# Kernel optimization log

Hardware: AMD Instinct MI355X
Metric: run time of the kernel (lower is better)

The kernel has to match this reference:

```python
import jax, jax.numpy as jnp
import numpy as np

N, E = 20000, 160000
NFEAT, NHID, NCLASS = 512, 256, 64


def _unif(key, shape):
    s = 1.0 / np.sqrt(shape[-1])
    return jax.random.uniform(key, shape, jnp.float32, -s, s)


def setup_inputs() -> dict:
    key = jax.random.key(0)
    ks = jax.random.split(key, 16)
    return {
        "x": jax.random.normal(ks[0], (N, NFEAT), jnp.float32),
        "edge_index": jax.random.randint(ks[1], (2, E), 0, N, dtype=jnp.int32).astype(jnp.int64),
        "head": 0,
        # Relation 1 (nfeat -> nfeat)
        "r1_g1": _unif(ks[2], (NFEAT, NFEAT)),
        "r1_g2": _unif(ks[3], (NFEAT, NFEAT)),
        "r1_b1": _unif(ks[4], (NFEAT, NFEAT)),
        "r1_b2": _unif(ks[5], (NFEAT, NFEAT)),
        "r1_m": _unif(ks[6], (1, NFEAT)),
        "gc1_w": _unif(ks[7], (NHID, NFEAT)),   # GCNConv.lin.weight [out,in]
        "gc1_b": jnp.zeros((NHID,), jnp.float32),
        # Relation 2 (nhid -> nhid)
        "r2_g1": _unif(ks[8], (NHID, NHID)),
        "r2_g2": _unif(ks[9], (NHID, NHID)),
        "r2_b1": _unif(ks[10], (NHID, NHID)),
        "r2_b2": _unif(ks[11], (NHID, NHID)),
        "r2_m": _unif(ks[12], (1, NHID)),
        "gc2_w": _unif(ks[13], (NCLASS, NHID)),
        "gc2_b": jnp.zeros((NCLASS,), jnp.float32),
    }


def _scatter_mean(vals, idx, n):
    s = jax.ops.segment_sum(vals, idx, num_segments=n)
    c = jax.ops.segment_sum(jnp.ones(idx.shape, vals.dtype), idx, num_segments=n)
    return s / jnp.clip(c, 1.0)[:, None]


def _relation(ft, nb, g1, g2, b1, b2, m):
    # gamma/beta FiLM-style modulation, then TransE-style translation
    gamma = jax.nn.leaky_relu(ft @ g1.T + nb @ g2.T, 0.2) + 1.0
    beta = jax.nn.leaky_relu(ft @ b1.T + nb @ b2.T, 0.2)
    return ft + (gamma * m + beta) - nb


def _gcn(x, edge_index, w, b):
    # PyG GCNConv with add_self_loops=True, symmetric normalization
    n = x.shape[0]
    h = x @ w.T
    loop = jnp.arange(n, dtype=edge_index.dtype)
    row = jnp.concatenate([edge_index[0], loop])
    col = jnp.concatenate([edge_index[1], loop])
    deg = jax.ops.segment_sum(jnp.ones(col.shape, h.dtype), col, num_segments=n)
    dinv = jnp.where(deg > 0, deg ** -0.5, 0.0)
    norm = dinv[row] * dinv[col]
    out = jax.ops.segment_sum(norm[:, None] * h[row], col, num_segments=n)
    return out + b


def _trans_gcn(x, edge_index, rg1, rg2, rb1, rb2, rm, gw, gb, head):
    row, col = edge_index[0], edge_index[1]
    n = x.shape[0]
    num_nb = jax.ops.segment_sum(jnp.ones(row.shape, x.dtype), row, num_segments=n)
    nb = _scatter_mean(x[col], row, n)
    output = _relation(x, nb, rg1, rg2, rb1, rb2, rm)
    h_k = _gcn(x, edge_index, gw, gb)
    if not head:  # tail branch (ablation=0: h_s = output)
        h_s = output @ gw.T
        h_k = (h_k + h_s) / (num_nb + 1.0)[:, None]
    return h_k, output


def reference(x, edge_index, head, r1_g1, r1_g2, r1_b1, r1_b2, r1_m, gc1_w, gc1_b,
              r2_g1, r2_g2, r2_b1, r2_b2, r2_m, gc2_w, gc2_b):
    x1, out1 = _trans_gcn(x, edge_index, r1_g1, r1_g2, r1_b1, r1_b2, r1_m, gc1_w, gc1_b, head)
    x1 = jax.nn.elu(x1)  # dropout is identity in eval mode
    x2, out2 = _trans_gcn(x1, edge_index, r2_g1, r2_g2, r2_b1, r2_b2, r2_m, gc2_w, gc2_b, head)
    return (x2, jax.nn.log_softmax(x2, axis=1), out1, out2)
```

## Files before the change

### kernel.cpp

```cpp
#include <hip/hip_runtime.h>
#include <hip/hip_bf16.h>
#include <stdint.h>

typedef __bf16 bf16;
typedef __attribute__((ext_vector_type(8))) __bf16 bf16x8;
typedef __attribute__((ext_vector_type(4))) float f32x4;

#define NNODE 20000
#define NEDGE 160000
#define NFEATD 512
#define NHIDD 256
#define NCLSD 64

__device__ __forceinline__ void async_copy16(const bf16* g, bf16* l) {
  __builtin_amdgcn_global_load_lds((__attribute__((address_space(1))) void*)g,
                                   (__attribute__((address_space(3))) void*)l,
                                   16, 0, 0);
}

struct GemmArgs {
  const bf16 *A1, *A2, *W1, *W2, *zpage;
  int ldA, ldW, K1, Ktot, Nvalid, ldC, Nrows, Arows, Wrows;
  bf16* outB;
  float* outF;
  float* outF2;
  const float* mrow;
  const float* Xf;
  const bf16* Xh;
  const bf16* nbm;
  float* outG;
  bf16* outB2;
  const float* agg;
  const bf16* hself;
  int hld;
  const float* dinv;
  const float* bias;
  const float* rnb;
  int elu;
  const bf16* Wh;
  int ldWh, Wrowsh, Kh, Nintmain;
};

template <int MODE>
__global__ __launch_bounds__(256) void gemm_bt(GemmArgs ga) {
  __shared__ bf16 sA[2][128 * 64];
  __shared__ bf16 sB[2][128 * 64];
  const int tid = threadIdx.x;
  const int lane = tid & 63;
  const int w = tid >> 6;
  const int wm = w >> 1, wn = w & 1;

  const int gx = gridDim.x;
  const int nwg = gx * gridDim.y;
  const int orig = blockIdx.y * gx + blockIdx.x;
  const int qq = nwg >> 3, rm = nwg & 7;
  const int xcd = orig & 7, sidx = orig >> 3;
  const int wg = (xcd < rm ? xcd * (qq + 1) : rm * (qq + 1) + (xcd - rm) * qq) + sidx;
  const int bn0 = (wg % gx) * 128;
  const int bm0 = (wg / gx) * 128;

  const bool isH = (MODE == 2) && ga.Wh && (bn0 >= ga.Nintmain);
  const bf16* Wp1 = isH ? ga.Wh : ga.W1;
  const bf16* Wp2 = isH ? ga.Wh : ga.W2;
  const int ldW = isH ? ga.ldWh : ga.ldW;
  const int Wrows = isH ? ga.Wrowsh : ga.Wrows;
  const int bn0L = isH ? bn0 - ga.Nintmain : bn0;
  const int nt1 = (isH ? ga.Kh : ga.K1) >> 6;
  const int nt = (isH ? ga.Kh : ga.Ktot) >> 6;

  const int srow = tid >> 3;
  const int scol = (((tid & 7) ^ (srow & 7)) << 3);
  const bf16* zp = ga.zpage + tid * 8;
  int offA[4], offB[4];
  bool okA[4], okB[4];
#pragma unroll
  for (int r = 0; r < 4; r++) {
    const int ra = bm0 + r * 32 + srow;
    const int rb = bn0L + r * 32 + srow;
    okA[r] = ra < ga.Arows;
    okB[r] = rb < Wrows;
    offA[r] = ra * ga.ldA + scol;
    offB[r] = rb * ldW + scol;
  }

  auto stage = [&](int t, int p) {
    const int seg = t >= nt1;
    const int koff = (t - (seg ? nt1 : 0)) << 6;
    const bf16* As = seg ? ga.A2 : ga.A1;
    const bf16* Ws = seg ? Wp2 : Wp1;
    bf16* dA = &sA[p][tid * 8];
    bf16* dB = &sB[p][tid * 8];
#pragma unroll
    for (int r = 0; r < 4; r++)
      async_copy16(okA[r] ? As + offA[r] + koff : zp, dA + r * 2048);
#pragma unroll
    for (int r = 0; r < 4; r++)
      async_copy16(okB[r] ? Ws + offB[r] + koff : zp, dB + r * 2048);
  };

  const int sl = lane >> 4;
  const int rAb = wm * 64 + (lane & 15);
  const int rBb = wn * 64 + (lane & 15);
  const int a7 = rAb & 7, b7 = rBb & 7;

  f32x4 acc[4][4] = {};

  stage(0, 0);
  stage(1, 1);
  asm volatile("s_waitcnt vmcnt(8)" ::: "memory");
  __builtin_amdgcn_s_barrier();
  asm volatile("" ::: "memory");

  for (int t = 0; t < nt; ++t) {
    const int p = t & 1;
    const bf16* pA = &sA[p][0];
    const bf16* pB = &sB[p][0];
    bf16x8 af[4][2], bv[4][2];
#pragma unroll
    for (int mi = 0; mi < 4; mi++)
#pragma unroll
      for (int kk = 0; kk < 2; kk++)
        af[mi][kk] = *(const bf16x8*)((const char*)pA + (rAb + mi * 16) * 128 +
                                      ((((kk << 2) + sl) ^ a7) << 4));
#pragma unroll
    for (int ni = 0; ni < 4; ni++)
#pragma unroll
      for (int kk = 0; kk < 2; kk++)
        bv[ni][kk] = *(const bf16x8*)((const char*)pB + (rBb + ni * 16) * 128 +
                                      ((((kk << 2) + sl) ^ b7) << 4));
    if (t + 2 < nt) {
      asm volatile("s_waitcnt lgkmcnt(0)" ::: "memory");
      __builtin_amdgcn_s_barrier();
      asm volatile("" ::: "memory");
      stage(t + 2, p);
    }
    __builtin_amdgcn_s_setprio(1);
#pragma unroll
    for (int mi = 0; mi < 4; mi++)
#pragma unroll
      for (int ni = 0; ni < 4; ni++)
#pragma unroll
        for (int kk = 0; kk < 2; kk++)
          acc[mi][ni] =
              __builtin_amdgcn_mfma_f32_16x16x32_bf16(af[mi][kk], bv[ni][kk], acc[mi][ni], 0, 0, 0);
    __builtin_amdgcn_s_setprio(0);
    if (t + 1 < nt) {
      if (t + 2 < nt) asm volatile("s_waitcnt vmcnt(8)" ::: "memory");
      else            asm volatile("s_waitcnt vmcnt(0)" ::: "memory");
      __builtin_amdgcn_s_barrier();
      asm volatile("" ::: "memory");
    }
  }

  if constexpr (MODE == 0) {
    const int Nv = ga.Nvalid;
#pragma unroll
    for (int mi = 0; mi < 4; mi++) {
      const int rb = bm0 + wm * 64 + mi * 16 + ((lane >> 4) << 2);
#pragma unroll
      for (int ni = 0; ni < 4; ni++) {
        const int c = bn0 + wn * 64 + ni * 16 + (lane & 15);
#pragma unroll
        for (int i = 0; i < 4; i++) {
          const int r = rb + i;
          if (r < ga.Nrows && c < Nv) ga.outB[(size_t)r * ga.ldC + c] = (bf16)acc[mi][ni][i];
        }
      }
    }
  } else if constexpr (MODE == 2) {
    if (isH) {
#pragma unroll
      for (int mi = 0; mi < 4; mi++) {
        const int rb = bm0 + wm * 64 + mi * 16 + ((lane >> 4) << 2);
#pragma unroll
        for (int ni = 0; ni < 4; ni++) {
          const int c = bn0L + wn * 64 + ni * 16 + (lane & 15);
#pragma unroll
          for (int i = 0; i < 4; i++) {
            const int r = rb + i;
            if (r < ga.Nrows && c < ga.ldC) ga.outB[(size_t)r * ga.ldC + c] = (bf16)acc[mi][ni][i];
          }
        }
      }
    } else {
      const int Dr = ga.Nvalid;
      const int Lb = ((bn0 + wn * 64) >> 1) + (lane & 15);
#pragma unroll
      for (int mi = 0; mi < 4; mi++) {
        const int rb = bm0 + wm * 64 + mi * 16 + ((lane >> 4) << 2);
#pragma unroll
        for (int p = 0; p < 2; p++) {
          const int L = Lb + p * 16;
          const float mv = ga.mrow[L];
#pragma unroll
          for (int i = 0; i < 4; i++) {
            const int r = rb + i;
            if (r >= ga.Nrows) continue;
            const size_t idx = (size_t)r * Dr + L;
            float vg = acc[mi][2 * p][i];
            float vb = acc[mi][2 * p + 1][i];
            float gamma = (vg > 0.f ? vg : 0.2f * vg) + 1.0f;
            float beta = vb > 0.f ? vb : 0.2f * vb;
            float ft = ga.Xf ? ga.Xf[idx] : (float)ga.Xh[idx];
            float o = ft + gamma * mv + beta - (float)ga.nbm[idx];
            ga.outG[idx] = o;
            ga.outB2[idx] = (bf16)o;
          }
        }
      }
    }
  } else if constexpr (MODE == 3) {
    const int Nv = ga.Nvalid;
#pragma unroll
    for (int mi = 0; mi < 4; mi++) {
      const int rb = bm0 + wm * 64 + mi * 16 + ((lane >> 4) << 2);
#pragma unroll
      for (int ni = 0; ni < 4; ni++) {
        const int c = bn0 + wn * 64 + ni * 16 + (lane & 15);
#pragma unroll
        for (int i = 0; i < 4; i++) {
          const int r = rb + i;
          if (r >= ga.Nrows || c >= Nv) continue;
          const size_t idx = (size_t)r * ga.ldC + c;
          float dv = ga.dinv[r];
          float hs = (float)ga.hself[(size_t)r * ga.hld + c];
          float hv = (ga.agg[idx] + dv * dv * hs + ga.bias[c] + acc[mi][ni][i]) * ga.rnb[r];
          if (ga.elu) hv = hv > 0.f ? hv : expm1f(hv);
          ga.outB[idx] = (bf16)hv;
        }
      }
    }
  } else {
    if (wn == 0) {
#pragma unroll
      for (int mi = 0; mi < 4; mi++) {
        const int rb = bm0 + wm * 64 + mi * 16 + ((lane >> 4) << 2);
#pragma unroll
        for (int i = 0; i < 4; i++) {
          const int r = rb + i;
          const bool ok = r < ga.Nrows;
          float dv = ok ? ga.dinv[r] : 0.f;
          float rn = ok ? ga.rnb[r] : 1.f;
          float hv[4];
#pragma unroll
          for (int ni = 0; ni < 4; ni++) {
            const int c = ni * 16 + (lane & 15);
            float hs = ok ? (float)ga.hself[(size_t)r * ga.hld + c] : 0.f;
            float ag = ok ? ga.agg[(size_t)r * 64 + c] : 0.f;
            hv[ni] = ok ? (ag + dv * dv * hs + ga.bias[c] + acc[mi][ni][i]) * rn : 0.f;
          }
          float mx = fmaxf(fmaxf(hv[0], hv[1]), fmaxf(hv[2], hv[3]));
          mx = fmaxf(mx, __shfl_xor(mx, 1));
          mx = fmaxf(mx, __shfl_xor(mx, 2));
          mx = fmaxf(mx, __shfl_xor(mx, 4));
          mx = fmaxf(mx, __shfl_xor(mx, 8));
          float s = expf(hv[0] - mx) + expf(hv[1] - mx) + expf(hv[2] - mx) + expf(hv[3] - mx);
          s += __shfl_xor(s, 1);
          s += __shfl_xor(s, 2);
          s += __shfl_xor(s, 4);
          s += __shfl_xor(s, 8);
          float ls = logf(s);
          if (ok) {
#pragma unroll
            for (int ni = 0; ni < 4; ni++) {
              const int c = ni * 16 + (lane & 15);
              ga.outF[(size_t)r * 64 + c] = hv[ni];
              ga.outF2[(size_t)r * 64 + c] = hv[ni] - mx - ls;
            }
          }
        }
      }
    }
  }
}

#define PREP_NB0 10000
#define PREP_NB1 10128
#define PREP_NB2 10144
#define PREP_NB3 11168
#define PREP_NB4 11424
#define PREP_NB5 11589

__device__ __forceinline__ void cvt4(const float* __restrict__ src, bf16* __restrict__ dst,
                                     int i) {
  float4 v = *(const float4*)(src + i);
  union { bf16 b[4]; uint2 u; } o;
  o.b[0] = (bf16)v.x; o.b[1] = (bf16)v.y; o.b[2] = (bf16)v.z; o.b[3] = (bf16)v.w;
  *(uint2*)(dst + i) = o.u;
}

__device__ __forceinline__ void relw4(const float* __restrict__ g1, const float* __restrict__ g2,
                                      const float* __restrict__ b1, const float* __restrict__ b2,
                                      bf16* __restrict__ dst, int D, int idx) {
  int R = idx / (2 * D), C = idx % (2 * D);
  int q = R >> 5, s = R & 31;
  int sr = q * 16 + (s & 15);
  const float* src = (s < 16) ? ((C < D) ? g1 : g2) : ((C < D) ? b1 : b2);
  int cc = (C < D) ? C : C - D;
  float4 v = *(const float4*)(src + (size_t)sr * D + cc);
  union { bf16 b[4]; uint2 u; } o;
  o.b[0] = (bf16)v.x; o.b[1] = (bf16)v.y; o.b[2] = (bf16)v.z; o.b[3] = (bf16)v.w;
  *(uint2*)(dst + (size_t)R * 2 * D + C) = o.u;
}

__global__ __launch_bounds__(256) void prep_all(
    const float* __restrict__ x, const float* __restrict__ gc1w, const float* __restrict__ gc2w,
    const float* __restrict__ r1g1, const float* __restrict__ r1g2,
    const float* __restrict__ r1b1, const float* __restrict__ r1b2,
    const float* __restrict__ r2g1, const float* __restrict__ r2g2,
    const float* __restrict__ r2b1, const float* __restrict__ r2b2,
    bf16* __restrict__ xb, bf16* __restrict__ wgc1, bf16* __restrict__ wgc2,
    bf16* __restrict__ Wrel1, bf16* __restrict__ Wrel2,
    int* __restrict__ icr, int* __restrict__ icc, int* __restrict__ zpage) {
  const int b = blockIdx.x;
  const int tid = threadIdx.x;
  if (b < PREP_NB0) {
    cvt4(x, xb, (b * 256 + tid) * 4);
  } else if (b < PREP_NB1) {
    cvt4(gc1w, wgc1, ((b - PREP_NB0) * 256 + tid) * 4);
  } else if (b < PREP_NB2) {
    cvt4(gc2w, wgc2, ((b - PREP_NB1) * 256 + tid) * 4);
  } else if (b < PREP_NB3) {
    relw4(r1g1, r1g2, r1b1, r1b2, Wrel1, 512, ((b - PREP_NB2) * 256 + tid) * 4);
  } else if (b < PREP_NB4) {
    relw4(r2g1, r2g2, r2b1, r2b2, Wrel2, 256, ((b - PREP_NB3) * 256 + tid) * 4);
  } else {
    int i = (b - PREP_NB4) * 256 + tid;
    if (i < NNODE) icr[i] = 0;
    else if (i < 2 * NNODE) icc[i - NNODE] = 0;
    else if (i < 2 * NNODE + 2048) zpage[i - 2 * NNODE] = 0;
  }
}

__global__ void count_int(const int* __restrict__ ei, int* cr, int* cc, int E) {
  int e = blockIdx.x * 256 + threadIdx.x;
  if (e < E) {
    atomicAdd(&cr[ei[e]], 1);
    atomicAdd(&cc[ei[E + e]], 1);
  }
}

__global__ void scan_excl2(const int* __restrict__ cr, const int* __restrict__ cc,
                           int* __restrict__ rptr, int* __restrict__ cptr,
                           int* __restrict__ curr, int* __restrict__ curc,
                           float* __restrict__ nbscale, float* __restrict__ rnb,
                           float* __restrict__ dinv, int n) {
  int t = threadIdx.x;
  {
    int b0 = blockIdx.x * (n / 2);
    for (int j = b0 + t; j < b0 + n / 2; j += 256) {
      float a = (float)cr[j];
      nbscale[j] = 1.0f / fmaxf(a, 1.0f);
      rnb[j] = 1.0f / (a + 1.0f);
      dinv[j] = rsqrtf((float)cc[j] + 1.0f);
    }
  }
  const int* cnt = blockIdx.x ? cc : cr;
  int* ptr = blockIdx.x ? cptr : rptr;
  int* cur = blockIdx.x ? curc : curr;
  __shared__ int part[256];
  int chunk = (n + 255) / 256;
  int base = t * chunk;
  int s = 0;
  for (int i = 0; i < chunk; i++) {
    int j = base + i;
    if (j < n) s += cnt[j];
  }
  part[t] = s;
  __syncthreads();
  if (t == 0) {
    int r = 0;
    for (int i = 0; i < 256; i++) { int v = part[i]; part[i] = r; r += v; }
    ptr[n] = r;
  }
  __syncthreads();
  int run = part[t];
  for (int i = 0; i < chunk; i++) {
    int j = base + i;
    if (j < n) {
      ptr[j] = run;
      cur[j] = run;
      run += cnt[j];
    }
  }
}

__global__ void csr_fill(const int* __restrict__ ei, int* cur_r, int* cur_c,
                         int* __restrict__ adj_r, int* __restrict__ adj_c, int E) {
  int e = blockIdx.x * 256 + threadIdx.x;
  if (e >= E) return;
  int row = ei[e], col = ei[E + e];
  int p = atomicAdd(&cur_r[row], 1);
  adj_r[p] = col;
  int q = atomicAdd(&cur_c[col], 1);
  adj_c[q] = row;
}

__global__ void spmm_nb1(const int* __restrict__ rowptr, const int* __restrict__ adj,
                         const bf16* __restrict__ x, const float* __restrict__ nbscale,
                         bf16* __restrict__ nbp, int n) {
  int r = blockIdx.x * 4 + (threadIdx.x >> 6);
  if (r >= n) return;
  int lane = threadIdx.x & 63;
  int e0 = rowptr[r], e1 = rowptr[r + 1];
  float a[8] = {0.f, 0.f, 0.f, 0.f, 0.f, 0.f, 0.f, 0.f};
  int e = e0;
  for (; e + 8 <= e1; e += 8) {
    union { uint4 u; bf16 b[8]; } v[8];
    int ix[8];
#pragma unroll
    for (int k = 0; k < 8; k++) ix[k] = adj[e + k];
#pragma unroll
    for (int k = 0; k < 8; k++) v[k].u = *(const uint4*)(x + (size_t)ix[k] * NFEATD + lane * 8);
#pragma unroll
    for (int j = 0; j < 8; j++) {
      float t = 0.f;
#pragma unroll
      for (int k = 0; k < 8; k++) t += (float)v[k].b[j];
      a[j] += t;
    }
  }
  for (; e + 4 <= e1; e += 4) {
    int i0 = adj[e], i1 = adj[e + 1], i2 = adj[e + 2], i3 = adj[e + 3];
    union { uint4 u; bf16 b[8]; } v0, v1, v2, v3;
    v0.u = *(const uint4*)(x + (size_t)i0 * NFEATD + lane * 8);
    v1.u = *(const uint4*)(x + (size_t)i1 * NFEATD + lane * 8);
    v2.u = *(const uint4*)(x + (size_t)i2 * NFEATD + lane * 8);
    v3.u = *(const uint4*)(x + (size_t)i3 * NFEATD + lane * 8);
#pragma unroll
    for (int j = 0; j < 8; j++)
      a[j] += (float)v0.b[j] + (float)v1.b[j] + (float)v2.b[j] + (float)v3.b[j];
  }
  for (; e < e1; e++) {
    union { uint4 u; bf16 b[8]; } v;
    v.u = *(const uint4*)(x + (size_t)adj[e] * NFEATD + lane * 8);
#pragma unroll
    for (int j = 0; j < 8; j++) a[j] += (float)v.b[j];
  }
  float s = nbscale[r];
  union { bf16 b[8]; uint4 u; } o;
#pragma unroll
  for (int j = 0; j < 8; j++) o.b[j] = (bf16)(a[j] * s);
  *(uint4*)(nbp + (size_t)r * NFEATD + lane * 8) = o.u;
}

__global__ void spmm_nb2(const int* __restrict__ rowptr, const int* __restrict__ adj,
                         const bf16* __restrict__ x, const float* __restrict__ nbscale,
                         bf16* __restrict__ nbp, int n) {
  int r = blockIdx.x * 4 + (threadIdx.x >> 6);
  if (r >= n) return;
  int lane = threadIdx.x & 63;
  int e0 = rowptr[r], e1 = rowptr[r + 1];
  float a[4] = {0.f, 0.f, 0.f, 0.f};
  int e = e0;
  for (; e + 8 <= e1; e += 8) {
    union { uint2 u; bf16 b[4]; } v[8];
    int ix[8];
#pragma unroll
    for (int k = 0; k < 8; k++) ix[k] = adj[e + k];
#pragma unroll
    for (int k = 0; k < 8; k++) v[k].u = *(const uint2*)(x + (size_t)ix[k] * NHIDD + lane * 4);
#pragma unroll
    for (int j = 0; j < 4; j++) {
      float t = 0.f;
#pragma unroll
      for (int k = 0; k < 8; k++) t += (float)v[k].b[j];
      a[j] += t;
    }
  }
  for (; e + 4 <= e1; e += 4) {
    int i0 = adj[e], i1 = adj[e + 1], i2 = adj[e + 2], i3 = adj[e + 3];
    union { uint2 u; bf16 b[4]; } v0, v1, v2, v3;
    v0.u = *(const uint2*)(x + (size_t)i0 * NHIDD + lane * 4);
    v1.u = *(const uint2*)(x + (size_t)i1 * NHIDD + lane * 4);
    v2.u = *(const uint2*)(x + (size_t)i2 * NHIDD + lane * 4);
    v3.u = *(const uint2*)(x + (size_t)i3 * NHIDD + lane * 4);
#pragma unroll
    for (int j = 0; j < 4; j++)
      a[j] += (float)v0.b[j] + (float)v1.b[j] + (float)v2.b[j] + (float)v3.b[j];
  }
  for (; e < e1; e++) {
    union { uint2 u; bf16 b[4]; } v;
    v.u = *(const uint2*)(x + (size_t)adj[e] * NHIDD + lane * 4);
#pragma unroll
    for (int j = 0; j < 4; j++) a[j] += (float)v.b[j];
  }
  float s = nbscale[r];
  union { bf16 b[4]; uint2 u; } o;
#pragma unroll
  for (int j = 0; j < 4; j++) o.b[j] = (bf16)(a[j] * s);
  *(uint2*)(nbp + (size_t)r * NHIDD + lane * 4) = o.u;
}

__global__ void spmm_gcn256(const int* __restrict__ colptr, const int* __restrict__ adj,
                            const bf16* __restrict__ h, int hld, const float* __restrict__ dinv,
                            float* __restrict__ agg, int n) {
  int c = blockIdx.x * 4 + (threadIdx.x >> 6);
  if (c >= n) return;
  int lane = threadIdx.x & 63;
  int e0 = colptr[c], e1 = colptr[c + 1];
  float a[4] = {0.f, 0.f, 0.f, 0.f};
  int e = e0;
  for (; e + 4 <= e1; e += 4) {
    int i0 = adj[e], i1 = adj[e + 1], i2 = adj[e + 2], i3 = adj[e + 3];
    float w0 = dinv[i0], w1 = dinv[i1], w2 = dinv[i2], w3 = dinv[i3];
    union { uint2 u; bf16 b[4]; } v0, v1, v2, v3;
    v0.u = *(const uint2*)(h + (size_t)i0 * hld + lane * 4);
    v1.u = *(const uint2*)(h + (size_t)i1 * hld + lane * 4);
    v2.u = *(const uint2*)(h + (size_t)i2 * hld + lane * 4);
    v3.u = *(const uint2*)(h + (size_t)i3 * hld + lane * 4);
#pragma unroll
    for (int j = 0; j < 4; j++)
      a[j] += w0 * (float)v0.b[j] + w1 * (float)v1.b[j] + w2 * (float)v2.b[j] + w3 * (float)v3.b[j];
  }
  for (; e < e1; e++) {
    int rr = adj[e];
    float wv = dinv[rr];
    union { uint2 u; bf16 b[4]; } v;
    v.u = *(const uint2*)(h + (size_t)rr * hld + lane * 4);
#pragma unroll
    for (int j = 0; j < 4; j++) a[j] += wv * (float)v.b[j];
  }
  float wc = dinv[c];
  f32x4 o;
#pragma unroll
  for (int j = 0; j < 4; j++) o[j] = a[j] * wc;
  *(f32x4*)(agg + (size_t)c * NHIDD + lane * 4) = o;
}

__global__ void spmm_gcn64(const int* __restrict__ colptr, const int* __restrict__ adj,
                           const bf16* __restrict__ h, int hld, const float* __restrict__ dinv,
                           float* __restrict__ agg, int n) {
  int c = blockIdx.x * 4 + (threadIdx.x >> 6);
  if (c >= n) return;
  int lane = threadIdx.x & 63;
  int e0 = colptr[c], e1 = colptr[c + 1];
  float a = 0.f;
  int e = e0;
  for (; e + 4 <= e1; e += 4) {
    int i0 = adj[e], i1 = adj[e + 1], i2 = adj[e + 2], i3 = adj[e + 3];
    float h0 = (float)h[(size_t)i0 * hld + lane];
    float h1 = (float)h[(size_t)i1 * hld + lane];
    float h2 = (float)h[(size_t)i2 * hld + lane];
    float h3 = (float)h[(size_t)i3 * hld + lane];
    a += dinv[i0] * h0 + dinv[i1] * h1 + dinv[i2] * h2 + dinv[i3] * h3;
  }
  for (; e < e1; e++) {
    int rr = adj[e];
    a += dinv[rr] * (float)h[(size_t)rr * hld + lane];
  }
  agg[(size_t)c * NCLSD + lane] = a * dinv[c];
}

extern "C" void kernel_launch(void* const* d_in, const int* in_sizes, int n_in, void* d_out,
                              int out_size, void* d_ws, size_t ws_size, hipStream_t stream) {
  const float* x = (const float*)d_in[0];
  const int* ei = (const int*)d_in[1];
  const float* r1g1 = (const float*)d_in[3];
  const float* r1g2 = (const float*)d_in[4];
  const float* r1b1 = (const float*)d_in[5];
  const float* r1b2 = (const float*)d_in[6];
  const float* r1m = (const float*)d_in[7];
  const float* gc1w = (const float*)d_in[8];
  const float* gc1b = (const float*)d_in[9];
  const float* r2g1 = (const float*)d_in[10];
  const float* r2g2 = (const float*)d_in[11];
  const float* r2b1 = (const float*)d_in[12];
  const float* r2b2 = (const float*)d_in[13];
  const float* r2m = (const float*)d_in[14];
  const float* gc2w = (const float*)d_in[15];
  const float* gc2b = (const float*)d_in[16];
  float* out = (float*)d_out;

  char* ws = (char*)d_ws;
  size_t off = 0;
  auto alloc = [&](size_t bytes) -> char* {
    char* p = ws + off;
    off = (off + bytes + 511) & ~(size_t)511;
    return p;
  };
  float* nbscale = (float*)alloc((size_t)NNODE * 4);
  float* rnb = (float*)alloc((size_t)NNODE * 4);
  float* dinv = (float*)alloc((size_t)NNODE * 4);
  int* icr = (int*)alloc((size_t)NNODE * 4);
  int* icc = (int*)alloc((size_t)NNODE * 4);
  int* rptr = (int*)alloc((size_t)(NNODE + 1) * 4);
  int* cptr = (int*)alloc((size_t)(NNODE + 1) * 4);
  int* curr = (int*)alloc((size_t)NNODE * 4);
  int* curc = (int*)alloc((size_t)NNODE * 4);
  int* adjr = (int*)alloc((size_t)NEDGE * 4);
  int* adjc = (int*)alloc((size_t)NEDGE * 4);
  bf16* zpage = (bf16*)alloc(8192);
  bf16* Wrel1 = (bf16*)alloc((size_t)1024 * 1024 * 2);
  bf16* Wrel2 = (bf16*)alloc((size_t)512 * 512 * 2);
  bf16* wgc1 = (bf16*)alloc((size_t)NHIDD * NFEATD * 2);
  bf16* wgc2 = (bf16*)alloc((size_t)NCLSD * NHIDD * 2);
  bf16* xb = (bf16*)alloc((size_t)NNODE * NFEATD * 2);
  bf16* nbp1 = (bf16*)alloc((size_t)NNODE * NFEATD * 2);
  bf16* out1b = (bf16*)alloc((size_t)NNODE * NFEATD * 2);
  bf16* h1b = (bf16*)alloc((size_t)NNODE * NHIDD * 2);
  float* agg1 = (float*)alloc((size_t)NNODE * NHIDD * 4);
  bf16* x1b = (bf16*)alloc((size_t)NNODE * NHIDD * 2);
  bf16* nb2p = (bf16*)alloc((size_t)NNODE * NHIDD * 2);
  bf16* out2b = (bf16*)alloc((size_t)NNODE * NHIDD * 2);
  bf16* h2b = (bf16*)alloc((size_t)NNODE * NCLSD * 2);
  float* agg2 = (float*)alloc((size_t)NNODE * NCLSD * 4);

  const size_t OUT1OFF = (size_t)2 * NNODE * NCLSD;
  const size_t OUT2OFF = OUT1OFF + (size_t)NNODE * NFEATD;
  float* out1g = out + OUT1OFF;
  float* out2g = out + OUT2OFF;

  const int MB = (NNODE + 127) / 128;
  const int NW4 = (NNODE + 3) / 4;

  prep_all<<<PREP_NB5, 256, 0, stream>>>(x, gc1w, gc2w, r1g1, r1g2, r1b1, r1b2,
                                         r2g1, r2g2, r2b1, r2b2, xb, wgc1, wgc2,
                                         Wrel1, Wrel2, icr, icc, (int*)zpage);

  count_int<<<(NEDGE + 255) / 256, 256, 0, stream>>>(ei, icr, icc, NEDGE);
  scan_excl2<<<2, 256, 0, stream>>>(icr, icc, rptr, cptr, curr, curc, nbscale, rnb, dinv, NNODE);
  csr_fill<<<(NEDGE + 255) / 256, 256, 0, stream>>>(ei, curr, curc, adjr, adjc, NEDGE);

  spmm_nb1<<<NW4, 256, 0, stream>>>(rptr, adjr, xb, nbscale, nbp1, NNODE);

  GemmArgs a;
  auto base = [&](const bf16* A1, const bf16* A2, int ldA, const bf16* W1, const bf16* W2,
                  int ldW, int K1, int Kt, int Nv, int ldC, int Wr) {
    a = GemmArgs{};
    a.A1 = A1; a.A2 = A2; a.W1 = W1; a.W2 = W2; a.zpage = zpage;
    a.ldA = ldA; a.ldW = ldW; a.K1 = K1; a.Ktot = Kt; a.Nvalid = Nv; a.ldC = ldC;
    a.Nrows = NNODE; a.Arows = NNODE; a.Wrows = Wr;
  };

  base(xb, nbp1, NFEATD, Wrel1, Wrel1 + 512, 1024, NFEATD, 2 * NFEATD, NFEATD, NHIDD, 1024);
  a.mrow = r1m; a.Xf = x; a.nbm = nbp1; a.outG = out1g; a.outB2 = out1b;
  a.Wh = wgc1; a.ldWh = NFEATD; a.Wrowsh = NHIDD; a.Kh = NFEATD; a.Nintmain = 1024;
  a.outB = h1b;
  gemm_bt<2><<<dim3(10, MB), 256, 0, stream>>>(a);

  spmm_gcn256<<<NW4, 256, 0, stream>>>(cptr, adjc, h1b, NHIDD, dinv, agg1, NNODE);

  base(out1b, out1b, NFEATD, wgc1, wgc1, NFEATD, NFEATD, NFEATD, NHIDD, NHIDD, NHIDD);
  a.agg = agg1; a.hself = h1b; a.hld = NHIDD; a.dinv = dinv; a.bias = gc1b; a.rnb = rnb;
  a.elu = 1; a.outB = x1b;
  gemm_bt<3><<<dim3(2, MB), 256, 0, stream>>>(a);

  spmm_nb2<<<NW4, 256, 0, stream>>>(rptr, adjr, x1b, nbscale, nb2p, NNODE);

  base(x1b, nb2p, NHIDD, Wrel2, Wrel2 + 256, 512, NHIDD, 2 * NHIDD, NHIDD, NCLSD, 512);
  a.mrow = r2m; a.Xf = nullptr; a.Xh = x1b; a.nbm = nb2p; a.outG = out2g; a.outB2 = out2b;
  a.Wh = wgc2; a.ldWh = NHIDD; a.Wrowsh = NCLSD; a.Kh = NHIDD; a.Nintmain = 512;
  a.outB = h2b;
  gemm_bt<2><<<dim3(5, MB), 256, 0, stream>>>(a);

  spmm_gcn64<<<NW4, 256, 0, stream>>>(cptr, adjc, h2b, NCLSD, dinv, agg2, NNODE);

  base(out2b, out2b, NHIDD, wgc2, wgc2, NHIDD, NHIDD, NHIDD, NCLSD, NCLSD, NCLSD);
  a.agg = agg2; a.hself = h2b; a.hld = NCLSD; a.dinv = dinv; a.bias = gc2b; a.rnb = rnb;
  a.elu = 0; a.outF = out; a.outF2 = out + (size_t)NNODE * NCLSD;
  gemm_bt<4><<<dim3(1, MB), 256, 0, stream>>>(a);
}
```

Baseline: 493.6 us.

## Co-schedule SpMM gathers with independent GEMMs in single launches

Reorders the dependency graph so each sparse gather runs in the same launch as an independent GEMM. Extra workgroups beyond the GEMM tiles do the gather: the X@Wgc1 GEMM now runs with the first neighbour-mean gather, and the GCN aggregation of h1 runs inside the relation GEMM. The same pairing is applied in layer 2. This removes four separate launches and lets memory-bound gathers overlap compute-bound tiles, at the cost of more register pressure in one fused kernel and possible load imbalance between the two kinds of blocks.

```diff
diff --git a/kernel.cpp b/kernel.cpp
--- a/kernel.cpp
+++ b/kernel.cpp
@@ -21,6 +21,7 @@
 struct GemmArgs {
   const bf16 *A1, *A2, *W1, *W2, *zpage;
   int ldA, ldW, K1, Ktot, Nvalid, ldC, Nrows, Arows, Wrows;
+  int gxG, nGemm;
   bf16* outB;
   float* outF;
   float* outF2;
@@ -37,37 +38,166 @@
   const float* bias;
   const float* rnb;
   int elu;
-  const bf16* Wh;
-  int ldWh, Wrowsh, Kh, Nintmain;
+  const int* gptr;
+  const int* gadj;
+  const bf16* gsrc;
+  bf16* gdstB;
+  float* gdstF;
+  const float* gnbs;
 };
 
-template <int MODE>
+template <int MODE, int GM, int GW>
 __global__ __launch_bounds__(256) void gemm_bt(GemmArgs ga) {
   __shared__ bf16 sA[2][128 * 64];
   __shared__ bf16 sB[2][128 * 64];
   const int tid = threadIdx.x;
+  const int orig = blockIdx.x;
+
+  if constexpr (GM == 1) {
+    if (orig >= ga.nGemm) {
+      const int r = (orig - ga.nGemm) * 4 + (tid >> 6);
+      if (r < NNODE) {
+        const int lane = tid & 63;
+        const int e0 = ga.gptr[r], e1 = ga.gptr[r + 1];
+        if constexpr (GW == 512) {
+          float a[8] = {};
+          int e = e0;
+          for (; e + 8 <= e1; e += 8) {
+            union { uint4 u; bf16 b[8]; } v[8];
+            int ix[8];
+#pragma unroll
+            for (int k = 0; k < 8; k++) ix[k] = ga.gadj[e + k];
+#pragma unroll
+            for (int k = 0; k < 8; k++)
+              v[k].u = *(const uint4*)(ga.gsrc + (size_t)ix[k] * 512 + lane * 8);
+#pragma unroll
+            for (int j = 0; j < 8; j++) {
+              float t = 0.f;
+#pragma unroll
+              for (int k = 0; k < 8; k++) t += (float)v[k].b[j];
+              a[j] += t;
+            }
+          }
+          for (; e < e1; e++) {
+            union { uint4 u; bf16 b[8]; } v;
+            v.u = *(const uint4*)(ga.gsrc + (size_t)ga.gadj[e] * 512 + lane * 8);
+#pragma unroll
+            for (int j = 0; j < 8; j++) a[j] += (float)v.b[j];
+          }
+          float s = ga.gnbs[r];
+          union { bf16 b[8]; uint4 u; } o;
+#pragma unroll
+          for (int j = 0; j < 8; j++) o.b[j] = (bf16)(a[j] * s);
+          *(uint4*)(ga.gdstB + (size_t)r * 512 + lane * 8) = o.u;
+        } else {
+          float a[4] = {};
+          int e = e0;
+          for (; e + 8 <= e1; e += 8) {
+            union { uint2 u; bf16 b[4]; } v[8];
+            int ix[8];
+#pragma unroll
+            for (int k = 0; k < 8; k++) ix[k] = ga.gadj[e + k];
+#pragma unroll
+            for (int k = 0; k < 8; k++)
+              v[k].u = *(const uint2*)(ga.gsrc + (size_t)ix[k] * 256 + lane * 4);
+#pragma unroll
+            for (int j = 0; j < 4; j++) {
+              float t = 0.f;
+#pragma unroll
+              for (int k = 0; k < 8; k++) t += (float)v[k].b[j];
+              a[j] += t;
+            }
+          }
+          for (; e < e1; e++) {
+            union { uint2 u; bf16 b[4]; } v;
+            v.u = *(const uint2*)(ga.gsrc + (size_t)ga.gadj[e] * 256 + lane * 4);
+#pragma unroll
+            for (int j = 0; j < 4; j++) a[j] += (float)v.b[j];
+          }
+          float s = ga.gnbs[r];
+          union { bf16 b[4]; uint2 u; } o;
+#pragma unroll
+          for (int j = 0; j < 4; j++) o.b[j] = (bf16)(a[j] * s);
+          *(uint2*)(ga.gdstB + (size_t)r * 256 + lane * 4) = o.u;
+        }
+      }
+      return;
+    }
+  } else if constexpr (GM == 2) {
+    if (orig >= ga.nGemm) {
+      const int r = (orig - ga.nGemm) * 4 + (tid >> 6);
+      if (r < NNODE) {
+        const int lane = tid & 63;
+        const int e0 = ga.gptr[r], e1 = ga.gptr[r + 1];
+        if constexpr (GW == 256) {
+          float a[4] = {};
+          int e = e0;
+          for (; e + 8 <= e1; e += 8) {
+            union { uint2 u; bf16 b[4]; } v[8];
+            int ix[8];
+            float wv[8];
+#pragma unroll
+            for (int k = 0; k < 8; k++) ix[k] = ga.gadj[e + k];
+#pragma unroll
+            for (int k = 0; k < 8; k++) wv[k] = ga.dinv[ix[k]];
+#pragma unroll
+            for (int k = 0; k < 8; k++)
+              v[k].u = *(const uint2*)(ga.gsrc + (size_t)ix[k] * 256 + lane * 4);
+#pragma unroll
+            for (int j = 0; j < 4; j++) {
+              float t = 0.f;
+#pragma unroll
+              for (int k = 0; k < 8; k++) t += wv[k] * (float)v[k].b[j];
+              a[j] += t;
+            }
+          }
+          for (; e < e1; e++) {
+            int i0 = ga.gadj[e];
+            float w0 = ga.dinv[i0];
+            union { uint2 u; bf16 b[4]; } v;
+            v.u = *(const uint2*)(ga.gsrc + (size_t)i0 * 256 + lane * 4);
+#pragma unroll
+            for (int j = 0; j < 4; j++) a[j] += w0 * (float)v.b[j];
+          }
+          float wc = ga.dinv[r];
+          f32x4 o;
+#pragma unroll
+          for (int j = 0; j < 4; j++) o[j] = a[j] * wc;
+          *(f32x4*)(ga.gdstF + (size_t)r * 256 + lane * 4) = o;
+        } else {
+          float a = 0.f;
+          int e = e0;
+          for (; e + 4 <= e1; e += 4) {
+            int i0 = ga.gadj[e], i1 = ga.gadj[e + 1], i2 = ga.gadj[e + 2], i3 = ga.gadj[e + 3];
+            float h0 = (float)ga.gsrc[(size_t)i0 * 64 + lane];
+            float h1 = (float)ga.gsrc[(size_t)i1 * 64 + lane];
+            float h2 = (float)ga.gsrc[(size_t)i2 * 64 + lane];
+            float h3 = (float)ga.gsrc[(size_t)i3 * 64 + lane];
+            a += ga.dinv[i0] * h0 + ga.dinv[i1] * h1 + ga.dinv[i2] * h2 + ga.dinv[i3] * h3;
+          }
+          for (; e < e1; e++) {
+            int rr = ga.gadj[e];
+            a += ga.dinv[rr] * (float)ga.gsrc[(size_t)rr * 64 + lane];
+          }
+          ga.gdstF[(size_t)r * 64 + lane] = a * ga.dinv[r];
+        }
+      }
+      return;
+    }
+  }
+
   const int lane = tid & 63;
   const int w = tid >> 6;
   const int wm = w >> 1, wn = w & 1;
 
-  const int gx = gridDim.x;
-  const int nwg = gx * gridDim.y;
-  const int orig = blockIdx.y * gx + blockIdx.x;
+  const int gx = ga.gxG;
+  const int nwg = ga.nGemm;
   const int qq = nwg >> 3, rm = nwg & 7;
   const int xcd = orig & 7, sidx = orig >> 3;
   const int wg = (xcd < rm ? xcd * (qq + 1) : rm * (qq + 1) + (xcd - rm) * qq) + sidx;
   const int bn0 = (wg % gx) * 128;
   const int bm0 = (wg / gx) * 128;
 
-  const bool isH = (MODE == 2) && ga.Wh && (bn0 >= ga.Nintmain);
-  const bf16* Wp1 = isH ? ga.Wh : ga.W1;
-  const bf16* Wp2 = isH ? ga.Wh : ga.W2;
-  const int ldW = isH ? ga.ldWh : ga.ldW;
-  const int Wrows = isH ? ga.Wrowsh : ga.Wrows;
-  const int bn0L = isH ? bn0 - ga.Nintmain : bn0;
-  const int nt1 = (isH ? ga.Kh : ga.K1) >> 6;
-  const int nt = (isH ? ga.Kh : ga.Ktot) >> 6;
-
   const int srow = tid >> 3;
   const int scol = (((tid & 7) ^ (srow & 7)) << 3);
   const bf16* zp = ga.zpage + tid * 8;
@@ -76,18 +206,20 @@
 #pragma unroll
   for (int r = 0; r < 4; r++) {
     const int ra = bm0 + r * 32 + srow;
-    const int rb = bn0L + r * 32 + srow;
+    const int rb = bn0 + r * 32 + srow;
     okA[r] = ra < ga.Arows;
-    okB[r] = rb < Wrows;
+    okB[r] = rb < ga.Wrows;
     offA[r] = ra * ga.ldA + scol;
-    offB[r] = rb * ldW + scol;
-  }
+    offB[r] = rb * ga.ldW + scol;
+  }
+  const int nt1 = ga.K1 >> 6;
+  const int nt = ga.Ktot >> 6;
 
   auto stage = [&](int t, int p) {
     const int seg = t >= nt1;
     const int koff = (t - (seg ? nt1 : 0)) << 6;
     const bf16* As = seg ? ga.A2 : ga.A1;
-    const bf16* Ws = seg ? Wp2 : Wp1;
+    const bf16* Ws = seg ? ga.W2 : ga.W1;
     bf16* dA = &sA[p][tid * 8];
     bf16* dB = &sB[p][tid * 8];
 #pragma unroll
@@ -168,44 +300,28 @@
       }
     }
   } else if constexpr (MODE == 2) {
-    if (isH) {
-#pragma unroll
-      for (int mi = 0; mi < 4; mi++) {
-        const int rb = bm0 + wm * 64 + mi * 16 + ((lane >> 4) << 2);
-#pragma unroll
-        for (int ni = 0; ni < 4; ni++) {
-          const int c = bn0L + wn * 64 + ni * 16 + (lane & 15);
-#pragma unroll
-          for (int i = 0; i < 4; i++) {
-            const int r = rb + i;
-            if (r < ga.Nrows && c < ga.ldC) ga.outB[(size_t)r * ga.ldC + c] = (bf16)acc[mi][ni][i];
-          }
-        }
-      }
-    } else {
-      const int Dr = ga.Nvalid;
-      const int Lb = ((bn0 + wn * 64) >> 1) + (lane & 15);
-#pragma unroll
-      for (int mi = 0; mi < 4; mi++) {
-        const int rb = bm0 + wm * 64 + mi * 16 + ((lane >> 4) << 2);
-#pragma unroll
-        for (int p = 0; p < 2; p++) {
-          const int L = Lb + p * 16;
-          const float mv = ga.mrow[L];
-#pragma unroll
-          for (int i = 0; i < 4; i++) {
-            const int r = rb + i;
-            if (r >= ga.Nrows) continue;
-            const size_t idx = (size_t)r * Dr + L;
-            float vg = acc[mi][2 * p][i];
-            float vb = acc[mi][2 * p + 1][i];
-            float gamma = (vg > 0.f ? vg : 0.2f * vg) + 1.0f;
-            float beta = vb > 0.f ? vb : 0.2f * vb;
-            float ft = ga.Xf ? ga.Xf[idx] : (float)ga.Xh[idx];
-            float o = ft + gamma * mv + beta - (float)ga.nbm[idx];
-            ga.outG[idx] = o;
-            ga.outB2[idx] = (bf16)o;
-          }
+    const int Dr = ga.Nvalid;
+    const int Lb = ((bn0 + wn * 64) >> 1) + (lane & 15);
+#pragma unroll
+    for (int mi = 0; mi < 4; mi++) {
+      const int rb = bm0 + wm * 64 + mi * 16 + ((lane >> 4) << 2);
+#pragma unroll
+      for (int p = 0; p < 2; p++) {
+        const int L = Lb + p * 16;
+        const float mv = ga.mrow[L];
+#pragma unroll
+        for (int i = 0; i < 4; i++) {
+          const int r = rb + i;
+          if (r >= ga.Nrows) continue;
+          const size_t idx = (size_t)r * Dr + L;
+          float vg = acc[mi][2 * p][i];
+          float vb = acc[mi][2 * p + 1][i];
+          float gamma = (vg > 0.f ? vg : 0.2f * vg) + 1.0f;
+          float beta = vb > 0.f ? vb : 0.2f * vb;
+          float ft = ga.Xf ? ga.Xf[idx] : (float)ga.Xh[idx];
+          float o = ft + gamma * mv + beta - (float)ga.nbm[idx];
+          ga.outG[idx] = o;
+          ga.outB2[idx] = (bf16)o;
         }
       }
     }
@@ -394,162 +510,6 @@
   adj_r[p] = col;
   int q = atomicAdd(&cur_c[col], 1);
   adj_c[q] = row;
-}
-
-__global__ void spmm_nb1(const int* __restrict__ rowptr, const int* __restrict__ adj,
-                         const bf16* __restrict__ x, const float* __restrict__ nbscale,
-                         bf16* __restrict__ nbp, int n) {
-  int r = blockIdx.x * 4 + (threadIdx.x >> 6);
-  if (r >= n) return;
-  int lane = threadIdx.x & 63;
-  int e0 = rowptr[r], e1 = rowptr[r + 1];
-  float a[8] = {0.f, 0.f, 0.f, 0.f, 0.f, 0.f, 0.f, 0.f};
-  int e = e0;
-  for (; e + 8 <= e1; e += 8) {
-    union { uint4 u; bf16 b[8]; } v[8];
-    int ix[8];
-#pragma unroll
-    for (int k = 0; k < 8; k++) ix[k] = adj[e + k];
-#pragma unroll
-    for (int k = 0; k < 8; k++) v[k].u = *(const uint4*)(x + (size_t)ix[k] * NFEATD + lane * 8);
-#pragma unroll
-    for (int j = 0; j < 8; j++) {
-      float t = 0.f;
-#pragma unroll
-      for (int k = 0; k < 8; k++) t += (float)v[k].b[j];
-      a[j] += t;
-    }
-  }
-  for (; e + 4 <= e1; e += 4) {
-    int i0 = adj[e], i1 = adj[e + 1], i2 = adj[e + 2], i3 = adj[e + 3];
-    union { uint4 u; bf16 b[8]; } v0, v1, v2, v3;
-    v0.u = *(const uint4*)(x + (size_t)i0 * NFEATD + lane * 8);
-    v1.u = *(const uint4*)(x + (size_t)i1 * NFEATD + lane * 8);
-    v2.u = *(const uint4*)(x + (size_t)i2 * NFEATD + lane * 8);
-    v3.u = *(const uint4*)(x + (size_t)i3 * NFEATD + lane * 8);
-#pragma unroll
-    for (int j = 0; j < 8; j++)
-      a[j] += (float)v0.b[j] + (float)v1.b[j] + (float)v2.b[j] + (float)v3.b[j];
-  }
-  for (; e < e1; e++) {
-    union { uint4 u; bf16 b[8]; } v;
-    v.u = *(const uint4*)(x + (size_t)adj[e] * NFEATD + lane * 8);
-#pragma unroll
-    for (int j = 0; j < 8; j++) a[j] += (float)v.b[j];
-  }
-  float s = nbscale[r];
-  union { bf16 b[8]; uint4 u; } o;
-#pragma unroll
-  for (int j = 0; j < 8; j++) o.b[j] = (bf16)(a[j] * s);
-  *(uint4*)(nbp + (size_t)r * NFEATD + lane * 8) = o.u;
-}
-
-__global__ void spmm_nb2(const int* __restrict__ rowptr, const int* __restrict__ adj,
-                         const bf16* __restrict__ x, const float* __restrict__ nbscale,
-                         bf16* __restrict__ nbp, int n) {
-  int r = blockIdx.x * 4 + (threadIdx.x >> 6);
-  if (r >= n) return;
-  int lane = threadIdx.x & 63;
-  int e0 = rowptr[r], e1 = rowptr[r + 1];
-  float a[4] = {0.f, 0.f, 0.f, 0.f};
-  int e = e0;
-  for (; e + 8 <= e1; e += 8) {
-    union { uint2 u; bf16 b[4]; } v[8];
-    int ix[8];
-#pragma unroll
-    for (int k = 0; k < 8; k++) ix[k] = adj[e + k];
-#pragma unroll
-    for (int k = 0; k < 8; k++) v[k].u = *(const uint2*)(x + (size_t)ix[k] * NHIDD + lane * 4);
-#pragma unroll
-    for (int j = 0; j < 4; j++) {
-      float t = 0.f;
-#pragma unroll
-      for (int k = 0; k < 8; k++) t += (float)v[k].b[j];
-      a[j] += t;
-    }
-  }
-  for (; e + 4 <= e1; e += 4) {
-    int i0 = adj[e], i1 = adj[e + 1], i2 = adj[e + 2], i3 = adj[e + 3];
-    union { uint2 u; bf16 b[4]; } v0, v1, v2, v3;
-    v0.u = *(const uint2*)(x + (size_t)i0 * NHIDD + lane * 4);
-    v1.u = *(const uint2*)(x + (size_t)i1 * NHIDD + lane * 4);
-    v2.u = *(const uint2*)(x + (size_t)i2 * NHIDD + lane * 4);
-    v3.u = *(const uint2*)(x + (size_t)i3 * NHIDD + lane * 4);
-#pragma unroll
-    for (int j = 0; j < 4; j++)
-      a[j] += (float)v0.b[j] + (float)v1.b[j] + (float)v2.b[j] + (float)v3.b[j];
-  }
-  for (; e < e1; e++) {
-    union { uint2 u; bf16 b[4]; } v;
-    v.u = *(const uint2*)(x + (size_t)adj[e] * NHIDD + lane * 4);
-#pragma unroll
-    for (int j = 0; j < 4; j++) a[j] += (float)v.b[j];
-  }
-  float s = nbscale[r];
-  union { bf16 b[4]; uint2 u; } o;
-#pragma unroll
-  for (int j = 0; j < 4; j++) o.b[j] = (bf16)(a[j] * s);
-  *(uint2*)(nbp + (size_t)r * NHIDD + lane * 4) = o.u;
-}
-
-__global__ void spmm_gcn256(const int* __restrict__ colptr, const int* __restrict__ adj,
-                            const bf16* __restrict__ h, int hld, const float* __restrict__ dinv,
-                            float* __restrict__ agg, int n) {
-  int c = blockIdx.x * 4 + (threadIdx.x >> 6);
-  if (c >= n) return;
-  int lane = threadIdx.x & 63;
-  int e0 = colptr[c], e1 = colptr[c + 1];
-  float a[4] = {0.f, 0.f, 0.f, 0.f};
-  int e = e0;
-  for (; e + 4 <= e1; e += 4) {
-    int i0 = adj[e], i1 = adj[e + 1], i2 = adj[e + 2], i3 = adj[e + 3];
-    float w0 = dinv[i0], w1 = dinv[i1], w2 = dinv[i2], w3 = dinv[i3];
-    union { uint2 u; bf16 b[4]; } v0, v1, v2, v3;
-    v0.u = *(const uint2*)(h + (size_t)i0 * hld + lane * 4);
-    v1.u = *(const uint2*)(h + (size_t)i1 * hld + lane * 4);
-    v2.u = *(const uint2*)(h + (size_t)i2 * hld + lane * 4);
-    v3.u = *(const uint2*)(h + (size_t)i3 * hld + lane * 4);
-#pragma unroll
-    for (int j = 0; j < 4; j++)
-      a[j] += w0 * (float)v0.b[j] + w1 * (float)v1.b[j] + w2 * (float)v2.b[j] + w3 * (float)v3.b[j];
-  }
-  for (; e < e1; e++) {
-    int rr = adj[e];
-    float wv = dinv[rr];
-    union { uint2 u; bf16 b[4]; } v;
-    v.u = *(const uint2*)(h + (size_t)rr * hld + lane * 4);
-#pragma unroll
-    for (int j = 0; j < 4; j++) a[j] += wv * (float)v.b[j];
-  }
-  float wc = dinv[c];
-  f32x4 o;
-#pragma unroll
-  for (int j = 0; j < 4; j++) o[j] = a[j] * wc;
-  *(f32x4*)(agg + (size_t)c * NHIDD + lane * 4) = o;
-}
-
-__global__ void spmm_gcn64(const int* __restrict__ colptr, const int* __restrict__ adj,
-                           const bf16* __restrict__ h, int hld, const float* __restrict__ dinv,
-                           float* __restrict__ agg, int n) {
-  int c = blockIdx.x * 4 + (threadIdx.x >> 6);
-  if (c >= n) return;
-  int lane = threadIdx.x & 63;
-  int e0 = colptr[c], e1 = colptr[c + 1];
-  float a = 0.f;
-  int e = e0;
-  for (; e + 4 <= e1; e += 4) {
-    int i0 = adj[e], i1 = adj[e + 1], i2 = adj[e + 2], i3 = adj[e + 3];
-    float h0 = (float)h[(size_t)i0 * hld + lane];
-    float h1 = (float)h[(size_t)i1 * hld + lane];
-    float h2 = (float)h[(size_t)i2 * hld + lane];
-    float h3 = (float)h[(size_t)i3 * hld + lane];
-    a += dinv[i0] * h0 + dinv[i1] * h1 + dinv[i2] * h2 + dinv[i3] * h3;
-  }
-  for (; e < e1; e++) {
-    int rr = adj[e];
-    a += dinv[rr] * (float)h[(size_t)rr * hld + lane];
-  }
-  agg[(size_t)c * NCLSD + lane] = a * dinv[c];
 }
 
 extern "C" void kernel_launch(void* const* d_in, const int* in_sizes, int n_in, void* d_out,
@@ -622,8 +582,6 @@
   scan_excl2<<<2, 256, 0, stream>>>(icr, icc, rptr, cptr, curr, curc, nbscale, rnb, dinv, NNODE);
   csr_fill<<<(NEDGE + 255) / 256, 256, 0, stream>>>(ei, curr, curc, adjr, adjc, NEDGE);
 
-  spmm_nb1<<<NW4, 256, 0, stream>>>(rptr, adjr, xb, nbscale, nbp1, NNODE);
-
   GemmArgs a;
   auto base = [&](const bf16* A1, const bf16* A2, int ldA, const bf16* W1, const bf16* W2,
                   int ldW, int K1, int Kt, int Nv, int ldC, int Wr) {
@@ -633,31 +591,36 @@
     a.Nrows = NNODE; a.Arows = NNODE; a.Wrows = Wr;
   };
 
-  base(xb, nbp1, NFEATD, Wrel1, Wrel1 + 512, 1024, NFEATD, 2 * NFEATD, NFEATD, NHIDD, 1024);
+  base(xb, xb, NFEATD, wgc1, wgc1, NFEATD, NFEATD, NFEATD, NHIDD, NHIDD, NHIDD);
+  a.outB = h1b; a.gxG = 2; a.nGemm = 2 * MB;
+  a.gptr = rptr; a.gadj = adjr; a.gsrc = xb; a.gdstB = nbp1; a.gnbs = nbscale;
+  gemm_bt<0, 1, 512><<<2 * MB + NW4, 256, 0, stream>>>(a);
+
+  base(xb, nbp1, NFEATD, Wrel1, Wrel1 + 512, 1024, NFEATD, 2 * NFEATD, NFEATD, NFEATD, 1024);
   a.mrow = r1m; a.Xf = x; a.nbm = nbp1; a.outG = out1g; a.outB2 = out1b;
-  a.Wh = wgc1; a.ldWh = NFEATD; a.Wrowsh = NHIDD; a.Kh = NFEATD; a.Nintmain = 1024;
-  a.outB = h1b;
-  gemm_bt<2><<<dim3(10, MB), 256, 0, stream>>>(a);
-
-  spmm_gcn256<<<NW4, 256, 0, stream>>>(cptr, adjc, h1b, NHIDD, dinv, agg1, NNODE);
+  a.gxG = 8; a.nGemm = 8 * MB;
+  a.gptr = cptr; a.gadj = adjc; a.gsrc = h1b; a.gdstF = agg1; a.dinv = dinv;
+  gemm_bt<2, 2, 256><<<8 * MB + NW4, 256, 0, stream>>>(a);
 
   base(out1b, out1b, NFEATD, wgc1, wgc1, NFEATD, NFEATD, NFEATD, NHIDD, NHIDD, NHIDD);
   a.agg = agg1; a.hself = h1b; a.hld = NHIDD; a.dinv = dinv; a.bias = gc1b; a.rnb = rnb;
-  a.elu = 1; a.outB = x1b;
-  gemm_bt<3><<<dim3(2, MB), 256, 0, stream>>>(a);
-
-  spmm_nb2<<<NW4, 256, 0, stream>>>(rptr, adjr, x1b, nbscale, nb2p, NNODE);
-
-  base(x1b, nb2p, NHIDD, Wrel2, Wrel2 + 256, 512, NHIDD, 2 * NHIDD, NHIDD, NCLSD, 512);
+  a.elu = 1; a.outB = x1b; a.gxG = 2; a.nGemm = 2 * MB;
+  gemm_bt<3, 0, 0><<<2 * MB, 256, 0, stream>>>(a);
+
+  base(x1b, x1b, NHIDD, wgc2, wgc2, NHIDD, NHIDD, NHIDD, NCLSD, NCLSD, NCLSD);
+  a.outB = h2b; a.gxG = 1; a.nGemm = MB;
+  a.gptr = rptr; a.gadj = adjr; a.gsrc = x1b; a.gdstB = nb2p; a.gnbs = nbscale;
+  gemm_bt<0, 1, 256><<<MB + NW4, 256, 0, stream>>>(a);
+
+  base(x1b, nb2p, NHIDD, Wrel2, Wrel2 + 256, 512, NHIDD, 2 * NHIDD, NHIDD, NHIDD, 512);
   a.mrow = r2m; a.Xf = nullptr; a.Xh = x1b; a.nbm = nb2p; a.outG = out2g; a.outB2 = out2b;
-  a.Wh = wgc2; a.ldWh = NHIDD; a.Wrowsh = NCLSD; a.Kh = NHIDD; a.Nintmain = 512;
-  a.outB = h2b;
-  gemm_bt<2><<<dim3(5, MB), 256, 0, stream>>>(a);
-
-  spmm_gcn64<<<NW4, 256, 0, stream>>>(cptr, adjc, h2b, NCLSD, dinv, agg2, NNODE);
+  a.gxG = 4; a.nGemm = 4 * MB;
+  a.gptr = cptr; a.gadj = adjc; a.gsrc = h2b; a.gdstF = agg2; a.dinv = dinv;
+  gemm_bt<2, 2, 64><<<4 * MB + NW4, 256, 0, stream>>>(a);
 
   base(out2b, out2b, NHIDD, wgc2, wgc2, NHIDD, NHIDD, NHIDD, NCLSD, NCLSD, NCLSD);
   a.agg = agg2; a.hself = h2b; a.hld = NCLSD; a.dinv = dinv; a.bias = gc2b; a.rnb = rnb;
   a.elu = 0; a.outF = out; a.outF2 = out + (size_t)NNODE * NCLSD;
-  gemm_bt<4><<<dim3(1, MB), 256, 0, stream>>>(a);
-}
+  a.gxG = 1; a.nGemm = MB;
+  gemm_bt<4, 0, 0><<<MB, 256, 0, stream>>>(a);
+}
```

New measurement: 563.8 us. 14.2% more time.
